# Kernel optimization log

Measured on AMD Instinct MI355X. Metric: run time of the kernel, lower is better.

## Reference

```python
import jax, jax.numpy as jnp
import numpy as np

N_NODES = 50000
N_EDGES = 1200000
D_FEAT = 64
HIDDEN = 32


def setup_inputs() -> dict:
    key = jax.random.key(0)
    ks = jax.random.split(key, 9)
    x = jax.random.normal(ks[0], (N_NODES, D_FEAT), dtype=jnp.float32)
    edge_index = jax.random.randint(ks[1], (2, N_EDGES), 0, N_NODES, dtype=jnp.int64)
    u = jax.random.normal(ks[2], (N_NODES,), dtype=jnp.float32)
    d_in = 2 * D_FEAT
    # MLP: Linear(d_in,H) -> relu -> Linear(H,H) -> relu -> Linear(H,1)
    W1 = jax.random.normal(ks[3], (d_in, HIDDEN), dtype=jnp.float32) / np.sqrt(d_in)
    b1 = jnp.zeros((HIDDEN,), dtype=jnp.float32)
    W2 = jax.random.normal(ks[4], (HIDDEN, HIDDEN), dtype=jnp.float32) / np.sqrt(HIDDEN)
    b2 = jnp.zeros((HIDDEN,), dtype=jnp.float32)
    W3 = jax.random.normal(ks[5], (HIDDEN, 1), dtype=jnp.float32) / np.sqrt(HIDDEN)
    b3 = jnp.zeros((1,), dtype=jnp.float32)
    return {"x": x, "edge_index": edge_index, "u": u,
            "W1": W1, "b1": b1, "W2": W2, "b2": b2, "W3": W3, "b3": b3}


def reference(x, edge_index, u, W1, b1, W2, b2, W3, b3):
    row, col = edge_index[0], edge_index[1]
    # gather + concat: [E, 2*D]
    x_edge = jnp.concatenate([x[row], x[col]], axis=-1)
    # per-edge MLP -> scalar weight per edge
    h = jax.nn.relu(x_edge @ W1 + b1)
    h = jax.nn.relu(h @ W2 + b2)
    edge_weight = (h @ W3 + b3)[:, 0]  # [E]
    # spmm: f[i] = sum_{e: row[e]==i} w_e * u[col[e]]
    f = jax.ops.segment_sum(edge_weight * u[col], row, num_segments=x.shape[0])
    return f
```

## Files before the change

### kernel.cpp

```cpp
#include <hip/hip_runtime.h>
#include <hip/hip_bf16.h>

#define N_NODES 50000
#define N_EDGES 1200000
#define D_FEAT  64
#define HIDDEN  32
#define N_TILES (N_NODES / 16)

typedef __attribute__((ext_vector_type(8))) short short8;
typedef __attribute__((ext_vector_type(4))) float floatx4;

__device__ __forceinline__ unsigned short f32_to_bf16(float f) {
    unsigned int u = __float_as_uint(f);
    unsigned int r = u + 0x7FFFu + ((u >> 16) & 1u);
    return (unsigned short)(r >> 16);
}
__device__ __forceinline__ float bf16_to_f32(unsigned short s) {
    return __uint_as_float(((unsigned int)s) << 16);
}

__global__ __launch_bounds__(256) void precompute_P_mfma(
    const float* __restrict__ x, const float* __restrict__ W1,
    const float* __restrict__ b1, unsigned short* __restrict__ P)
{
    const int lane = threadIdx.x & 63;
    const int n = lane & 15;
    const int q = lane >> 4;

    short8 bf[4][2];
    #pragma unroll
    for (int G = 0; G < 4; ++G) {
        #pragma unroll
        for (int h = 0; h < 2; ++h) {
            #pragma unroll
            for (int i = 0; i < 8; ++i) {
                const int k = h * 32 + q * 8 + i;
                const int j = n + 16 * G;
                const float w = (G < 2) ? W1[k * 32 + j]
                                        : W1[(64 + k) * 32 + (j - 32)];
                bf[G][h][i] = (short)f32_to_bf16(w);
            }
        }
    }
    const float binit[4] = { b1[n], b1[n + 16], 0.0f, 0.0f };

    const int tile = blockIdx.x * 4 + (int)(threadIdx.x >> 6);
    if (tile >= N_TILES) return;
    const int node = tile * 16 + n;

    const float4* xr = (const float4*)(x + (size_t)node * 64 + q * 8);
    float4 xa = xr[0], xb = xr[1];
    const float4* xr2 = (const float4*)(x + (size_t)node * 64 + 32 + q * 8);
    float4 xc = xr2[0], xd = xr2[1];

    short8 a0, a1;
    a0[0] = (short)f32_to_bf16(xa.x); a0[1] = (short)f32_to_bf16(xa.y);
    a0[2] = (short)f32_to_bf16(xa.z); a0[3] = (short)f32_to_bf16(xa.w);
    a0[4] = (short)f32_to_bf16(xb.x); a0[5] = (short)f32_to_bf16(xb.y);
    a0[6] = (short)f32_to_bf16(xb.z); a0[7] = (short)f32_to_bf16(xb.w);
    a1[0] = (short)f32_to_bf16(xc.x); a1[1] = (short)f32_to_bf16(xc.y);
    a1[2] = (short)f32_to_bf16(xc.z); a1[3] = (short)f32_to_bf16(xc.w);
    a1[4] = (short)f32_to_bf16(xd.x); a1[5] = (short)f32_to_bf16(xd.y);
    a1[6] = (short)f32_to_bf16(xd.z); a1[7] = (short)f32_to_bf16(xd.w);

    #pragma unroll
    for (int G = 0; G < 4; ++G) {
        floatx4 acc = { binit[G], binit[G], binit[G], binit[G] };
        acc = __builtin_amdgcn_mfma_f32_16x16x32_bf16(a0, bf[G][0], acc, 0, 0, 0);
        acc = __builtin_amdgcn_mfma_f32_16x16x32_bf16(a1, bf[G][1], acc, 0, 0, 0);
        #pragma unroll
        for (int r = 0; r < 4; ++r)
            P[(size_t)(tile * 16 + q * 4 + r) * 64 + n + 16 * G] =
                f32_to_bf16(acc[r]);
    }
}

__global__ __launch_bounds__(256) void edge_mlp_mfma(
    const int* __restrict__ row, const int* __restrict__ col,
    const float* __restrict__ u,
    const float* __restrict__ W2, const float* __restrict__ b2,
    const float* __restrict__ W3, const float* __restrict__ b3,
    const unsigned short* __restrict__ P, float* __restrict__ out)
{
    const int lane = threadIdx.x & 63;
    const int n = lane & 15;
    const int q = lane >> 4;

    short8 bf0, bf1;
    #pragma unroll
    for (int i = 0; i < 8; ++i) {
        const int k = q * 8 + i;
        bf0[i] = (short)f32_to_bf16(W2[k * 32 + n]);
        bf1[i] = (short)f32_to_bf16(W2[k * 32 + n + 16]);
    }
    const float w3n0 = W3[n], w3n1 = W3[n + 16];
    const float b2n0 = b2[n], b2n1 = b2[n + 16];
    const float bias3 = b3[0];

    const int wave   = (blockIdx.x * 256 + (int)threadIdx.x) >> 6;
    const int nwaves = gridDim.x * 4;
    const int nchunks = N_EDGES / 32;

    for (int ch = wave; ch < nchunks; ch += nwaves) {
        const int base0 = ch * 32;

        int rI[2], cI[2];
        #pragma unroll
        for (int t = 0; t < 2; ++t) {
            const int e = base0 + t * 16 + n;
            rI[t] = row[e];
            cI[t] = col[e];
        }
        int r2 = 0; float u2 = 0.0f;
        if (n < 8) {
            const int e2 = base0 + 16 * (n >> 2) + 4 * q + (n & 3);
            r2 = row[e2];
            u2 = u[col[e2]];
        }
        short8 v1[2], v2[2];
        #pragma unroll
        for (int t = 0; t < 2; ++t) {
            v1[t] = *(const short8*)(P + (size_t)rI[t] * 64 + q * 8);
            v2[t] = *(const short8*)(P + (size_t)cI[t] * 64 + 32 + q * 8);
        }

        float tr[2][4];
        #pragma unroll
        for (int t = 0; t < 2; ++t) {
            short8 a;
            #pragma unroll
            for (int i = 0; i < 8; ++i) {
                const float f1 = bf16_to_f32((unsigned short)v1[t][i]);
                const float f2 = bf16_to_f32((unsigned short)v2[t][i]);
                a[i] = (short)f32_to_bf16(fmaxf(f1 + f2, 0.0f));
            }
            floatx4 d0 = {b2n0, b2n0, b2n0, b2n0};
            floatx4 d1 = {b2n1, b2n1, b2n1, b2n1};
            d0 = __builtin_amdgcn_mfma_f32_16x16x32_bf16(a, bf0, d0, 0, 0, 0);
            d1 = __builtin_amdgcn_mfma_f32_16x16x32_bf16(a, bf1, d1, 0, 0, 0);
            #pragma unroll
            for (int r = 0; r < 4; ++r)
                tr[t][r] = fmaxf(d0[r], 0.0f) * w3n0 + fmaxf(d1[r], 0.0f) * w3n1;
        }

        #pragma unroll
        for (int mask = 1; mask < 16; mask <<= 1) {
            #pragma unroll
            for (int t = 0; t < 2; ++t)
                #pragma unroll
                for (int r = 0; r < 4; ++r)
                    tr[t][r] += __shfl_xor(tr[t][r], mask, 64);
        }

        if (n < 8) {
            const float va0 = (n & 4) ? tr[1][0] : tr[0][0];
            const float va1 = (n & 4) ? tr[1][1] : tr[0][1];
            const float va2 = (n & 4) ? tr[1][2] : tr[0][2];
            const float va3 = (n & 4) ? tr[1][3] : tr[0][3];
            const float vb0 = (n & 2) ? va2 : va0;
            const float vb1 = (n & 2) ? va3 : va1;
            const float v   = (n & 1) ? vb1 : vb0;
            atomicAdd(out + r2, (v + bias3) * u2);
        }
    }
}

extern "C" void kernel_launch(void* const* d_in, const int* in_sizes, int n_in,
                              void* d_out, int out_size, void* d_ws, size_t ws_size,
                              hipStream_t stream)
{
    const float* x    = (const float*)d_in[0];
    const int*   eidx = (const int*)  d_in[1];
    const float* u    = (const float*)d_in[2];
    const float* W1   = (const float*)d_in[3];
    const float* b1   = (const float*)d_in[4];
    const float* W2   = (const float*)d_in[5];
    const float* b2   = (const float*)d_in[6];
    const float* W3   = (const float*)d_in[7];
    const float* b3   = (const float*)d_in[8];

    const int* row = eidx;
    const int* col = eidx + N_EDGES;

    unsigned short* P = (unsigned short*)d_ws;
    float* out = (float*)d_out;

    hipMemsetAsync(out, 0, N_NODES * sizeof(float), stream);

    precompute_P_mfma<<<(N_TILES + 3) / 4, 256, 0, stream>>>(x, W1, b1, P);

    edge_mlp_mfma<<<1024, 256, 0, stream>>>(
        row, col, u, W2, b2, W3, b3, P, out);
}
```

Baseline: 160.5 us.

## Replicate output atomics across buffers, stage W1 in LDS, pack P stores

The edge kernel scatters its atomic adds into 16 replicated output arrays selected by wave index, and a new kernel sums the replicas into the output. This is meant to reduce atomic contention on popular nodes. The node precompute now stages a bf16 transposed W1 in shared memory, loops over tiles, and writes P as packed bf16 pairs, with W2 rows permuted to match. The cost is a larger memset and an extra reduction launch.

```diff
diff --git a/kernel.cpp b/kernel.cpp
--- a/kernel.cpp
+++ b/kernel.cpp
@@ -1,11 +1,11 @@
 #include <hip/hip_runtime.h>
-#include <hip/hip_bf16.h>
 
 #define N_NODES 50000
 #define N_EDGES 1200000
-#define D_FEAT  64
-#define HIDDEN  32
 #define N_TILES (N_NODES / 16)
+#define N_REP   16
+#define REP_STRIDE 50064
+#define W1T_STRIDE 72
 
 typedef __attribute__((ext_vector_type(8))) short short8;
 typedef __attribute__((ext_vector_type(4))) float floatx4;
@@ -18,60 +18,72 @@
 __device__ __forceinline__ float bf16_to_f32(unsigned short s) {
     return __uint_as_float(((unsigned int)s) << 16);
 }
+__device__ __forceinline__ unsigned int pack_bf16x2(float lo, float hi) {
+    return (unsigned int)f32_to_bf16(lo) | ((unsigned int)f32_to_bf16(hi) << 16);
+}
 
 __global__ __launch_bounds__(256) void precompute_P_mfma(
     const float* __restrict__ x, const float* __restrict__ W1,
     const float* __restrict__ b1, unsigned short* __restrict__ P)
 {
-    const int lane = threadIdx.x & 63;
+    __shared__ unsigned short W1t[64 * W1T_STRIDE];
+    const int tid = threadIdx.x;
+    for (int e = tid; e < 128 * 32; e += 256) {
+        const int kp = e >> 5, jp = e & 31;
+        const int k = kp & 63;
+        const int j = (kp < 64) ? jp : jp + 32;
+        W1t[j * W1T_STRIDE + k] = f32_to_bf16(W1[e]);
+    }
+    __syncthreads();
+
+    const int lane = tid & 63;
     const int n = lane & 15;
     const int q = lane >> 4;
 
     short8 bf[4][2];
     #pragma unroll
-    for (int G = 0; G < 4; ++G) {
-        #pragma unroll
-        for (int h = 0; h < 2; ++h) {
-            #pragma unroll
-            for (int i = 0; i < 8; ++i) {
-                const int k = h * 32 + q * 8 + i;
-                const int j = n + 16 * G;
-                const float w = (G < 2) ? W1[k * 32 + j]
-                                        : W1[(64 + k) * 32 + (j - 32)];
-                bf[G][h][i] = (short)f32_to_bf16(w);
-            }
-        }
-    }
-    const float binit[4] = { b1[n], b1[n + 16], 0.0f, 0.0f };
-
-    const int tile = blockIdx.x * 4 + (int)(threadIdx.x >> 6);
-    if (tile >= N_TILES) return;
-    const int node = tile * 16 + n;
-
-    const float4* xr = (const float4*)(x + (size_t)node * 64 + q * 8);
-    float4 xa = xr[0], xb = xr[1];
-    const float4* xr2 = (const float4*)(x + (size_t)node * 64 + 32 + q * 8);
-    float4 xc = xr2[0], xd = xr2[1];
-
-    short8 a0, a1;
-    a0[0] = (short)f32_to_bf16(xa.x); a0[1] = (short)f32_to_bf16(xa.y);
-    a0[2] = (short)f32_to_bf16(xa.z); a0[3] = (short)f32_to_bf16(xa.w);
-    a0[4] = (short)f32_to_bf16(xb.x); a0[5] = (short)f32_to_bf16(xb.y);
-    a0[6] = (short)f32_to_bf16(xb.z); a0[7] = (short)f32_to_bf16(xb.w);
-    a1[0] = (short)f32_to_bf16(xc.x); a1[1] = (short)f32_to_bf16(xc.y);
-    a1[2] = (short)f32_to_bf16(xc.z); a1[3] = (short)f32_to_bf16(xc.w);
-    a1[4] = (short)f32_to_bf16(xd.x); a1[5] = (short)f32_to_bf16(xd.y);
-    a1[6] = (short)f32_to_bf16(xd.z); a1[7] = (short)f32_to_bf16(xd.w);
-
-    #pragma unroll
-    for (int G = 0; G < 4; ++G) {
-        floatx4 acc = { binit[G], binit[G], binit[G], binit[G] };
-        acc = __builtin_amdgcn_mfma_f32_16x16x32_bf16(a0, bf[G][0], acc, 0, 0, 0);
-        acc = __builtin_amdgcn_mfma_f32_16x16x32_bf16(a1, bf[G][1], acc, 0, 0, 0);
-        #pragma unroll
-        for (int r = 0; r < 4; ++r)
-            P[(size_t)(tile * 16 + q * 4 + r) * 64 + n + 16 * G] =
-                f32_to_bf16(acc[r]);
+    for (int G = 0; G < 4; ++G)
+        #pragma unroll
+        for (int h = 0; h < 2; ++h)
+            bf[G][h] = *(const short8*)&W1t[(n + 16 * G) * W1T_STRIDE + h * 32 + q * 8];
+
+    const float bias0 = b1[n], bias1 = b1[n + 16];
+
+    unsigned int* P32 = (unsigned int*)P;
+
+    const int wid0   = blockIdx.x * 4 + (tid >> 6);
+    const int stride = gridDim.x * 4;
+    for (int tile = wid0; tile < N_TILES; tile += stride) {
+        const int node = tile * 16 + n;
+        const float4* xp  = (const float4*)(x + (size_t)node * 64 + q * 8);
+        const float4 xa = xp[0], xb = xp[1];
+        const float4* xp2 = (const float4*)(x + (size_t)node * 64 + 32 + q * 8);
+        const float4 xc = xp2[0], xd = xp2[1];
+
+        short8 a0, a1;
+        a0[0] = (short)f32_to_bf16(xa.x); a0[1] = (short)f32_to_bf16(xa.y);
+        a0[2] = (short)f32_to_bf16(xa.z); a0[3] = (short)f32_to_bf16(xa.w);
+        a0[4] = (short)f32_to_bf16(xb.x); a0[5] = (short)f32_to_bf16(xb.y);
+        a0[6] = (short)f32_to_bf16(xb.z); a0[7] = (short)f32_to_bf16(xb.w);
+        a1[0] = (short)f32_to_bf16(xc.x); a1[1] = (short)f32_to_bf16(xc.y);
+        a1[2] = (short)f32_to_bf16(xc.z); a1[3] = (short)f32_to_bf16(xc.w);
+        a1[4] = (short)f32_to_bf16(xd.x); a1[5] = (short)f32_to_bf16(xd.y);
+        a1[6] = (short)f32_to_bf16(xd.z); a1[7] = (short)f32_to_bf16(xd.w);
+
+        floatx4 acc[4];
+        #pragma unroll
+        for (int G = 0; G < 4; ++G) {
+            const float bi = (G == 0) ? bias0 : (G == 1) ? bias1 : 0.0f;
+            acc[G] = (floatx4){bi, bi, bi, bi};
+            acc[G] = __builtin_amdgcn_mfma_f32_16x16x32_bf16(a0, bf[G][0], acc[G], 0, 0, 0);
+            acc[G] = __builtin_amdgcn_mfma_f32_16x16x32_bf16(a1, bf[G][1], acc[G], 0, 0, 0);
+        }
+        #pragma unroll
+        for (int r = 0; r < 4; ++r) {
+            const int nr = tile * 16 + q * 4 + r;
+            P32[(size_t)nr * 32 + n]      = pack_bf16x2(acc[0][r], acc[1][r]);
+            P32[(size_t)nr * 32 + 16 + n] = pack_bf16x2(acc[2][r], acc[3][r]);
+        }
     }
 }
 
@@ -80,7 +92,7 @@
     const float* __restrict__ u,
     const float* __restrict__ W2, const float* __restrict__ b2,
     const float* __restrict__ W3, const float* __restrict__ b3,
-    const unsigned short* __restrict__ P, float* __restrict__ out)
+    const unsigned short* __restrict__ P, float* __restrict__ rep)
 {
     const int lane = threadIdx.x & 63;
     const int n = lane & 15;
@@ -89,9 +101,9 @@
     short8 bf0, bf1;
     #pragma unroll
     for (int i = 0; i < 8; ++i) {
-        const int k = q * 8 + i;
-        bf0[i] = (short)f32_to_bf16(W2[k * 32 + n]);
-        bf1[i] = (short)f32_to_bf16(W2[k * 32 + n + 16]);
+        const int F = q * 4 + (i >> 1) + 16 * (i & 1);
+        bf0[i] = (short)f32_to_bf16(W2[F * 32 + n]);
+        bf1[i] = (short)f32_to_bf16(W2[F * 32 + n + 16]);
     }
     const float w3n0 = W3[n], w3n1 = W3[n + 16];
     const float b2n0 = b2[n], b2n1 = b2[n + 16];
@@ -100,6 +112,7 @@
     const int wave   = (blockIdx.x * 256 + (int)threadIdx.x) >> 6;
     const int nwaves = gridDim.x * 4;
     const int nchunks = N_EDGES / 32;
+    float* myrep = rep + (size_t)(wave & (N_REP - 1)) * REP_STRIDE;
 
     for (int ch = wave; ch < nchunks; ch += nwaves) {
         const int base0 = ch * 32;
@@ -160,8 +173,21 @@
             const float vb0 = (n & 2) ? va2 : va0;
             const float vb1 = (n & 2) ? va3 : va1;
             const float v   = (n & 1) ? vb1 : vb0;
-            atomicAdd(out + r2, (v + bias3) * u2);
-        }
+            atomicAdd(myrep + r2, (v + bias3) * u2);
+        }
+    }
+}
+
+__global__ __launch_bounds__(256) void reduce_out(
+    const float* __restrict__ rep, float* __restrict__ out)
+{
+    const int i = blockIdx.x * 256 + (int)threadIdx.x;
+    if (i < N_NODES) {
+        float s = 0.0f;
+        #pragma unroll
+        for (int r = 0; r < N_REP; ++r)
+            s += rep[(size_t)r * REP_STRIDE + i];
+        out[i] = s;
     }
 }
 
@@ -183,12 +209,15 @@
     const int* col = eidx + N_EDGES;
 
     unsigned short* P = (unsigned short*)d_ws;
+    float* rep = (float*)((char*)d_ws + (size_t)N_NODES * 128);
     float* out = (float*)d_out;
 
-    hipMemsetAsync(out, 0, N_NODES * sizeof(float), stream);
-
-    precompute_P_mfma<<<(N_TILES + 3) / 4, 256, 0, stream>>>(x, W1, b1, P);
+    hipMemsetAsync(rep, 0, (size_t)N_REP * REP_STRIDE * sizeof(float), stream);
+
+    precompute_P_mfma<<<512, 256, 0, stream>>>(x, W1, b1, P);
 
     edge_mlp_mfma<<<1024, 256, 0, stream>>>(
-        row, col, u, W2, b2, W3, b3, P, out);
-}
+        row, col, u, W2, b2, W3, b3, P, rep);
+
+    reduce_out<<<(N_NODES + 255) / 256, 256, 0, stream>>>(rep, out);
+}
```

Result: faster. 153.1 us (-4.6%).
